# Kernel optimization log

Measured on AMD Instinct MI355X. Metric: run time of the kernel, lower is better.

## Reference

```python
import jax, jax.numpy as jnp
import numpy as np

BATCH = 64
IN_VECN = 1024
IN_VECL = 64
OUT_VECN = 64
OUT_VECL = 32
ROUTINGS = 3
EPS = 1e-5


def squash(x, axis=-1, eps=EPS):
    # squash(x) = |x|^2/(1+|x|^2) * x/(|x|+eps), matching the torch source
    n = jnp.linalg.norm(x, axis=axis, keepdims=True)
    n2 = n * n
    return n2 / (1.0 + n2) * x / (n + eps)


def setup_inputs() -> dict:
    key = jax.random.key(0)
    k1, k2, k3 = jax.random.split(key, 3)
    stdv = 1.0 / np.sqrt(IN_VECN * IN_VECL)  # reset_parameters: uniform(-stdv, stdv)
    u = jax.random.normal(k1, (BATCH, IN_VECN, IN_VECL), dtype=jnp.float32)
    weight = jax.random.uniform(k2, (IN_VECN, OUT_VECN, OUT_VECL, IN_VECL),
                                dtype=jnp.float32, minval=-stdv, maxval=stdv)
    bias = jax.random.uniform(k3, (IN_VECN, OUT_VECN, OUT_VECL),
                              dtype=jnp.float32, minval=-stdv, maxval=stdv)
    return {"u": u, "weight": weight, "bias": bias}


def reference(u, weight, bias):
    # u: [B, N, I]; weight: [N, O, L, I]; bias: [N, O, L]
    # u_hat: [B, N, O, L] -- per-input-capsule prediction for each output capsule
    u_hat = jnp.einsum('bni,noli->bnol', u, weight) + bias[None]
    # retain_grad=False: routing uses detached u_hat
    ud = jax.lax.stop_gradient(u_hat)
    # initial c = softmax(zeros) over out_vecn -> uniform 1/O, shape [1,1,O,1]
    c = jnp.full((1, 1, OUT_VECN, 1), 1.0 / OUT_VECN, dtype=u.dtype)
    b = jnp.zeros((u.shape[0], IN_VECN, OUT_VECN, 1), dtype=u.dtype)
    for _ in range(ROUTINGS - 1):
        v = squash(jnp.sum(ud * c, axis=-3), axis=-1)        # [B, O, L]
        b = b + jnp.sum(ud * v[:, None], axis=-1, keepdims=True)  # [B, N, O, 1]
        c = jax.nn.softmax(b, axis=-2)                        # softmax over O
    return squash(jnp.sum(u_hat * c, axis=-3), axis=-1)      # [B, O, L]
```

## Files before the change

kernel.cpp:

```cpp
#include <hip/hip_runtime.h>
#include <hip/hip_bf16.h>

#define BATCH 64
#define NIN 1024
#define IVL 64
#define ONUM 64
#define LVL 32
#define OLSZ 2048

typedef __attribute__((ext_vector_type(4))) float f32x4;
typedef __attribute__((ext_vector_type(8))) short short8;

static __device__ __forceinline__ unsigned short f2bf(float f) {
  unsigned u = __builtin_bit_cast(unsigned, f);
  u += 0x7fffu + ((u >> 16) & 1u);
  return (unsigned short)(u >> 16);
}
static __device__ __forceinline__ float bf2f_lo(unsigned x) {
  return __builtin_bit_cast(float, x << 16);
}
static __device__ __forceinline__ float bf2f_hi(unsigned x) {
  return __builtin_bit_cast(float, x & 0xffff0000u);
}

#define W_BURST(W, q0, q1, q2, q3)                                       \
  asm volatile(                                                          \
      "global_load_dwordx4 %[w0], %[a0], off\n\t"                        \
      "global_load_dwordx4 %[w1], %[a0], off offset:16\n\t"              \
      "global_load_dwordx4 %[w2], %[a0], off offset:128\n\t"             \
      "global_load_dwordx4 %[w3], %[a0], off offset:144\n\t"             \
      "global_load_dwordx4 %[w4], %[a1], off\n\t"                        \
      "global_load_dwordx4 %[w5], %[a1], off offset:16\n\t"              \
      "global_load_dwordx4 %[w6], %[a1], off offset:128\n\t"             \
      "global_load_dwordx4 %[w7], %[a1], off offset:144\n\t"             \
      "global_load_dwordx4 %[w8], %[a2], off\n\t"                        \
      "global_load_dwordx4 %[w9], %[a2], off offset:16\n\t"              \
      "global_load_dwordx4 %[w10], %[a2], off offset:128\n\t"            \
      "global_load_dwordx4 %[w11], %[a2], off offset:144\n\t"            \
      "global_load_dwordx4 %[w12], %[a3], off\n\t"                       \
      "global_load_dwordx4 %[w13], %[a3], off offset:16\n\t"             \
      "global_load_dwordx4 %[w14], %[a3], off offset:128\n\t"            \
      "global_load_dwordx4 %[w15], %[a3], off offset:144\n\t"            \
      : [w0] "=&v"(W[0]), [w1] "=&v"(W[1]), [w2] "=&v"(W[2]),            \
        [w3] "=&v"(W[3]), [w4] "=&v"(W[4]), [w5] "=&v"(W[5]),            \
        [w6] "=&v"(W[6]), [w7] "=&v"(W[7]), [w8] "=&v"(W[8]),            \
        [w9] "=&v"(W[9]), [w10] "=&v"(W[10]), [w11] "=&v"(W[11]),        \
        [w12] "=&v"(W[12]), [w13] "=&v"(W[13]), [w14] "=&v"(W[14]),      \
        [w15] "=&v"(W[15])                                               \
      : [a0] "v"(q0), [a1] "v"(q1), [a2] "v"(q2), [a3] "v"(q3)           \
      : "memory")

#define STORE16(P, s0, s1, s2, s3)                                       \
  asm volatile(                                                          \
      "global_store_dwordx2 %[a0], %[d0], off\n\t"                       \
      "global_store_dwordx2 %[a0], %[d1], off offset:32\n\t"             \
      "global_store_dwordx2 %[a0], %[d2], off offset:64\n\t"             \
      "global_store_dwordx2 %[a0], %[d3], off offset:96\n\t"             \
      "global_store_dwordx2 %[a1], %[d4], off\n\t"                       \
      "global_store_dwordx2 %[a1], %[d5], off offset:32\n\t"             \
      "global_store_dwordx2 %[a1], %[d6], off offset:64\n\t"             \
      "global_store_dwordx2 %[a1], %[d7], off offset:96\n\t"             \
      "global_store_dwordx2 %[a2], %[d8], off\n\t"                       \
      "global_store_dwordx2 %[a2], %[d9], off offset:32\n\t"             \
      "global_store_dwordx2 %[a2], %[d10], off offset:64\n\t"            \
      "global_store_dwordx2 %[a2], %[d11], off offset:96\n\t"            \
      "global_store_dwordx2 %[a3], %[d12], off\n\t"                      \
      "global_store_dwordx2 %[a3], %[d13], off offset:32\n\t"            \
      "global_store_dwordx2 %[a3], %[d14], off offset:64\n\t"            \
      "global_store_dwordx2 %[a3], %[d15], off offset:96\n\t"            \
      :: [a0] "v"(s0), [a1] "v"(s1), [a2] "v"(s2), [a3] "v"(s3),         \
         [d0] "v"(P[0]), [d1] "v"(P[1]), [d2] "v"(P[2]), [d3] "v"(P[3]), \
         [d4] "v"(P[4]), [d5] "v"(P[5]), [d6] "v"(P[6]), [d7] "v"(P[7]), \
         [d8] "v"(P[8]), [d9] "v"(P[9]), [d10] "v"(P[10]),               \
         [d11] "v"(P[11]), [d12] "v"(P[12]), [d13] "v"(P[13]),           \
         [d14] "v"(P[14]), [d15] "v"(P[15])                              \
      : "memory")

#define VMWAIT16                                        \
  do {                                                  \
    asm volatile("s_waitcnt vmcnt(16)" ::: "memory");   \
    __builtin_amdgcn_sched_barrier(0);                  \
  } while (0)
#define VMWAIT0                                         \
  do {                                                  \
    asm volatile("s_waitcnt vmcnt(0)" ::: "memory");    \
    __builtin_amdgcn_sched_barrier(0);                  \
  } while (0)

__global__ __launch_bounds__(256, 2) void k_gemm(
    const float* __restrict__ u, const float* __restrict__ w,
    const float* __restrict__ bias, unsigned short* __restrict__ uhat) {
  const int n = blockIdx.x;
  const int half = blockIdx.y;
  __shared__ __align__(16) unsigned short a_lds[64 * 72];
  __shared__ __align__(16) float bias_lds[1024];
  const int t = threadIdx.x;
  const int lane = t & 63;
  const int wave = t >> 6;
  const int row16 = lane & 15;
  const int quad = lane >> 4;

  {
    const int b = t >> 2;
    const int i0 = (t & 3) * 16;
    const float* src = u + (size_t)b * (NIN * IVL) + (size_t)n * IVL + i0;
    unsigned short* dst = a_lds + b * 72 + i0;
#pragma unroll
    for (int q = 0; q < 4; ++q) {
      float4 v = *(const float4*)(src + q * 4);
      dst[q * 4 + 0] = f2bf(v.x);
      dst[q * 4 + 1] = f2bf(v.y);
      dst[q * 4 + 2] = f2bf(v.z);
      dst[q * 4 + 3] = f2bf(v.w);
    }
    *(float4*)&bias_lds[t * 4] =
        *(const float4*)(bias + (size_t)n * OLSZ + half * 1024 + t * 4);
  }
  __syncthreads();

  short8 uf[4][2];
#pragma unroll
  for (int bt = 0; bt < 4; ++bt) {
#pragma unroll
    for (int ks = 0; ks < 2; ++ks) {
      uf[bt][ks] =
          *(const short8*)(a_lds + (bt * 16 + row16) * 72 + ks * 32 + quad * 8);
    }
  }
  asm volatile("s_waitcnt lgkmcnt(0)" ::: "memory");
  __builtin_amdgcn_sched_barrier(0);

  const float* wp = w + (size_t)n * (OLSZ * IVL) +
                    (size_t)(half * 1024 + wave * 64 + row16) * IVL + quad * 8;
  const float* p0 = wp;
  const float* p1 = wp + 16 * IVL;
  const float* p2 = wp + 32 * IVL;
  const float* p3 = wp + 48 * IVL;
  const unsigned short* sb0 =
      uhat + ((size_t)(0 * 16 + row16) * NIN + n) * OLSZ + half * 1024 +
      wave * 64 + quad * 4;
  const unsigned short* sb1 = sb0 + (size_t)16 * NIN * OLSZ;
  const unsigned short* sb2 = sb0 + (size_t)32 * NIN * OLSZ;
  const unsigned short* sb3 = sb0 + (size_t)48 * NIN * OLSZ;

  f32x4 wvA[16], wvB[16];

#define COMPUTE_STORE(W, c)                                                   \
  do {                                                                        \
    uint2 pks[16];                                                            \
    _Pragma("unroll") for (int tile = 0; tile < 4; ++tile) {                  \
      const f32x4 A0 = W[tile * 4 + 0];                                       \
      const f32x4 A1 = W[tile * 4 + 1];                                       \
      const f32x4 A2 = W[tile * 4 + 2];                                       \
      const f32x4 A3 = W[tile * 4 + 3];                                       \
      short8 wf0, wf1;                                                        \
      wf0[0] = (short)f2bf(A0[0]); wf0[1] = (short)f2bf(A0[1]);               \
      wf0[2] = (short)f2bf(A0[2]); wf0[3] = (short)f2bf(A0[3]);               \
      wf0[4] = (short)f2bf(A1[0]); wf0[5] = (short)f2bf(A1[1]);               \
      wf0[6] = (short)f2bf(A1[2]); wf0[7] = (short)f2bf(A1[3]);               \
      wf1[0] = (short)f2bf(A2[0]); wf1[1] = (short)f2bf(A2[1]);               \
      wf1[2] = (short)f2bf(A2[2]); wf1[3] = (short)f2bf(A2[3]);               \
      wf1[4] = (short)f2bf(A3[0]); wf1[5] = (short)f2bf(A3[1]);               \
      wf1[6] = (short)f2bf(A3[2]); wf1[7] = (short)f2bf(A3[3]);               \
      float4 bf = *(const float4*)&bias_lds[(c) * 256 + wave * 64 +           \
                                            tile * 16 + quad * 4];            \
      f32x4 acc0 = (f32x4){0.f, 0.f, 0.f, 0.f};                               \
      f32x4 acc1 = acc0, acc2 = acc0, acc3 = acc0;                            \
      acc0 = __builtin_amdgcn_mfma_f32_16x16x32_bf16(wf0, uf[0][0], acc0, 0, 0, 0); \
      acc0 = __builtin_amdgcn_mfma_f32_16x16x32_bf16(wf1, uf[0][1], acc0, 0, 0, 0); \
      acc1 = __builtin_amdgcn_mfma_f32_16x16x32_bf16(wf0, uf[1][0], acc1, 0, 0, 0); \
      acc1 = __builtin_amdgcn_mfma_f32_16x16x32_bf16(wf1, uf[1][1], acc1, 0, 0, 0); \
      acc2 = __builtin_amdgcn_mfma_f32_16x16x32_bf16(wf0, uf[2][0], acc2, 0, 0, 0); \
      acc2 = __builtin_amdgcn_mfma_f32_16x16x32_bf16(wf1, uf[2][1], acc2, 0, 0, 0); \
      acc3 = __builtin_amdgcn_mfma_f32_16x16x32_bf16(wf0, uf[3][0], acc3, 0, 0, 0); \
      acc3 = __builtin_amdgcn_mfma_f32_16x16x32_bf16(wf1, uf[3][1], acc3, 0, 0, 0); \
      pks[0 * 4 + tile] = make_uint2(                                         \
          f2bf(acc0[0] + bf.x) | (f2bf(acc0[1] + bf.y) << 16),                \
          f2bf(acc0[2] + bf.z) | (f2bf(acc0[3] + bf.w) << 16));               \
      pks[1 * 4 + tile] = make_uint2(                                         \
          f2bf(acc1[0] + bf.x) | (f2bf(acc1[1] + bf.y) << 16),                \
          f2bf(acc1[2] + bf.z) | (f2bf(acc1[3] + bf.w) << 16));               \
      pks[2 * 4 + tile] = make_uint2(                                         \
          f2bf(acc2[0] + bf.x) | (f2bf(acc2[1] + bf.y) << 16),                \
          f2bf(acc2[2] + bf.z) | (f2bf(acc2[3] + bf.w) << 16));               \
      pks[3 * 4 + tile] = make_uint2(                                         \
          f2bf(acc3[0] + bf.x) | (f2bf(acc3[1] + bf.y) << 16),                \
          f2bf(acc3[2] + bf.z) | (f2bf(acc3[3] + bf.w) << 16));               \
    }                                                                         \
    const unsigned short* s0 = sb0 + (c) * 256;                               \
    const unsigned short* s1 = sb1 + (c) * 256;                               \
    const unsigned short* s2 = sb2 + (c) * 256;                               \
    const unsigned short* s3 = sb3 + (c) * 256;                               \
    STORE16(pks, s0, s1, s2, s3);                                             \
  } while (0)

  W_BURST(wvA, p0, p1, p2, p3);
  W_BURST(wvB, p0 + 16384, p1 + 16384, p2 + 16384, p3 + 16384);
  VMWAIT16;
  COMPUTE_STORE(wvA, 0);
  W_BURST(wvA, p0 + 32768, p1 + 32768, p2 + 32768, p3 + 32768);
  VMWAIT16;
  COMPUTE_STORE(wvB, 1);
  W_BURST(wvB, p0 + 49152, p1 + 49152, p2 + 49152, p3 + 49152);
  VMWAIT16;
  COMPUTE_STORE(wvA, 2);
  VMWAIT0;
  COMPUTE_STORE(wvB, 3);
#undef COMPUTE_STORE
}

__global__ __launch_bounds__(256) void k_sum_n(
    const unsigned short* __restrict__ uhat, float* __restrict__ s1) {
  const int b = blockIdx.x >> 5;
  const int chunk = blockIdx.x & 31;
  const int t = threadIdx.x;
  const unsigned short* base =
      uhat + ((size_t)b * NIN + (size_t)chunk * 32) * OLSZ + t * 8;
  float acc[8];
#pragma unroll
  for (int j = 0; j < 8; ++j) acc[j] = 0.f;
#pragma unroll 4
  for (int k = 0; k < 32; ++k) {
    uint4 p = *(const uint4*)(base + (size_t)k * OLSZ);
    unsigned xs[4] = {p.x, p.y, p.z, p.w};
#pragma unroll
    for (int h = 0; h < 4; ++h) {
      acc[2 * h] += bf2f_lo(xs[h]);
      acc[2 * h + 1] += bf2f_hi(xs[h]);
    }
  }
  float* s = s1 + (size_t)b * OLSZ + t * 8;
#pragma unroll
  for (int j = 0; j < 8; ++j) atomicAdd(s + j, acc[j]);
}

__global__ __launch_bounds__(256) void k_route(
    const unsigned short* __restrict__ uhat, const float* __restrict__ sv,
    float scale, float* __restrict__ b1, int add_b1,
    float* __restrict__ sout) {
  const int b = blockIdx.x >> 5;
  const int chunk = blockIdx.x & 31;
  const int t = threadIdx.x;
  const int lane = t & 63;
  const int wave = t >> 6;
  const int g = lane >> 2;
  __shared__ float red[4][OLSZ];

  float v[4][8];
#pragma unroll
  for (int q = 0; q < 4; ++q) {
    const float* svp = sv + (size_t)b * OLSZ + q * 512 + lane * 8;
    float4 a0 = *(const float4*)svp;
    float4 a1 = *(const float4*)(svp + 4);
    v[q][0] = a0.x * scale; v[q][1] = a0.y * scale;
    v[q][2] = a0.z * scale; v[q][3] = a0.w * scale;
    v[q][4] = a1.x * scale; v[q][5] = a1.y * scale;
    v[q][6] = a1.z * scale; v[q][7] = a1.w * scale;
    float p = 0.f;
#pragma unroll
    for (int j = 0; j < 8; ++j) p = fmaf(v[q][j], v[q][j], p);
    p += __shfl_xor(p, 1);
    p += __shfl_xor(p, 2);
    float f = p / ((1.f + p) * (sqrtf(p) + 1e-5f));
#pragma unroll
    for (int j = 0; j < 8; ++j) v[q][j] *= f;
  }

  float racc[4][8];
#pragma unroll
  for (int q = 0; q < 4; ++q)
#pragma unroll
    for (int j = 0; j < 8; ++j) racc[q][j] = 0.f;

  const int n0 = chunk * 32 + wave * 8;
  const unsigned short* ub = uhat + ((size_t)b * NIN + n0) * OLSZ + lane * 8;

  uint4 pA[4], pB[4];
#pragma unroll
  for (int q = 0; q < 4; ++q) pA[q] = *(const uint4*)(ub + q * 512);

  auto process = [&](const uint4(&pk)[4], int k) {
    const int n = n0 + k;
    const size_t bbase = ((size_t)b * NIN + n) * ONUM + g;
    float b1v[4];
    if (add_b1) {
#pragma unroll
      for (int q = 0; q < 4; ++q) b1v[q] = b1[bbase + 16 * q];
    }
    float ud[4][8];
    float d[4];
#pragma unroll
    for (int q = 0; q < 4; ++q) {
      unsigned xs[4] = {pk[q].x, pk[q].y, pk[q].z, pk[q].w};
#pragma unroll
      for (int h = 0; h < 4; ++h) {
        ud[q][2 * h] = bf2f_lo(xs[h]);
        ud[q][2 * h + 1] = bf2f_hi(xs[h]);
      }
      float p = 0.f;
#pragma unroll
      for (int j = 0; j < 8; ++j) p = fmaf(ud[q][j], v[q][j], p);
      p += __shfl_xor(p, 1);
      p += __shfl_xor(p, 2);
      d[q] = p;
    }
    float bno[4];
    if (add_b1) {
#pragma unroll
      for (int q = 0; q < 4; ++q) bno[q] = d[q] + b1v[q];
    } else {
#pragma unroll
      for (int q = 0; q < 4; ++q) bno[q] = d[q];
      if ((lane & 3) == 0) {
#pragma unroll
        for (int q = 0; q < 4; ++q) b1[bbase + 16 * q] = d[q];
      }
    }
    float m = fmaxf(fmaxf(bno[0], bno[1]), fmaxf(bno[2], bno[3]));
#pragma unroll
    for (int dl = 4; dl < 64; dl <<= 1) m = fmaxf(m, __shfl_xor(m, dl));
    float e0 = __expf(bno[0] - m);
    float e1 = __expf(bno[1] - m);
    float e2 = __expf(bno[2] - m);
    float e3 = __expf(bno[3] - m);
    float ls = (e0 + e1) + (e2 + e3);
#pragma unroll
    for (int dl = 4; dl < 64; dl <<= 1) ls += __shfl_xor(ls, dl);
    float inv = 1.0f / ls;
    float c[4] = {e0 * inv, e1 * inv, e2 * inv, e3 * inv};
#pragma unroll
    for (int q = 0; q < 4; ++q) {
#pragma unroll
      for (int j = 0; j < 8; ++j)
        racc[q][j] = fmaf(c[q], ud[q][j], racc[q][j]);
    }
  };

#pragma unroll
  for (int kk = 0; kk < 4; ++kk) {
    {
#pragma unroll
      for (int q = 0; q < 4; ++q)
        pB[q] = *(const uint4*)(ub + (size_t)(2 * kk + 1) * OLSZ + q * 512);
    }
    process(pA, 2 * kk);
    if (2 * kk + 2 < 8) {
#pragma unroll
      for (int q = 0; q < 4; ++q)
        pA[q] = *(const uint4*)(ub + (size_t)(2 * kk + 2) * OLSZ + q * 512);
    }
    process(pB, 2 * kk + 1);
  }

#pragma unroll
  for (int q = 0; q < 4; ++q) {
    float* dst = &red[wave][q * 512 + lane * 8];
    *(float4*)(dst) =
        make_float4(racc[q][0], racc[q][1], racc[q][2], racc[q][3]);
    *(float4*)(dst + 4) =
        make_float4(racc[q][4], racc[q][5], racc[q][6], racc[q][7]);
  }
  __syncthreads();
  float* so = sout + (size_t)b * OLSZ;
#pragma unroll
  for (int j = 0; j < 8; ++j) {
    const int idx = t + 256 * j;
    float s = (red[0][idx] + red[1][idx]) + (red[2][idx] + red[3][idx]);
    atomicAdd(so + idx, s);
  }
}

__global__ __launch_bounds__(256) void k_final(const float* __restrict__ s3,
                                               float* __restrict__ out) {
  const int b = blockIdx.x;
  const int t = threadIdx.x;
  __shared__ float norm2[64];
  if (t < 64) norm2[t] = 0.f;
  __syncthreads();
  float scv[8];
#pragma unroll
  for (int k = 0; k < 8; ++k) {
    int idx = t + k * 256;
    float sc = s3[b * OLSZ + idx];
    scv[k] = sc;
    atomicAdd(&norm2[idx >> 5], sc * sc);
  }
  __syncthreads();
#pragma unroll
  for (int k = 0; k < 8; ++k) {
    int idx = t + k * 256;
    int o = idx >> 5;
    float n2 = norm2[o];
    float f = n2 / ((1.f + n2) * (sqrtf(n2) + 1e-5f));
    out[b * OLSZ + idx] = scv[k] * f;
  }
}

extern "C" void kernel_launch(void* const* d_in, const int* in_sizes, int n_in,
                              void* d_out, int out_size, void* d_ws,
                              size_t ws_size, hipStream_t stream) {
  const float* u = (const float*)d_in[0];
  const float* w = (const float*)d_in[1];
  const float* bias = (const float*)d_in[2];
  float* out = (float*)d_out;

  char* ws = (char*)d_ws;
  unsigned short* uhat = (unsigned short*)ws;
  float* b1 = (float*)(ws + (size_t)268435456);
  float* s1 = (float*)(ws + (size_t)268435456 + 16777216);
  float* s2 = s1 + 131072;
  float* s3 = s2 + 131072;

  hipMemsetAsync(s1, 0, 3 * 131072 * sizeof(float), stream);

  k_gemm<<<dim3(1024, 2), dim3(256), 0, stream>>>(u, w, bias, uhat);
  k_sum_n<<<dim3(2048), dim3(256), 0, stream>>>(uhat, s1);
  k_route<<<dim3(2048), dim3(256), 0, stream>>>(uhat, s1, 1.0f / 64.0f, b1, 0, s2);
  k_route<<<dim3(2048), dim3(256), 0, stream>>>(uhat, s2, 1.0f, b1, 1, s3);
  k_final<<<dim3(64), dim3(256), 0, stream>>>(s3, out);
}
```

Before: 492.1 us.

## Restructure GEMM weight pipeline into smaller bursts and fold memset into kernel

The gemm kernel now streams weights in 8-load bursts over eight double-buffered steps instead of 16-load bursts over four. Each wave now owns a contiguous 256-output span, so stores use immediate offsets from fixed base pointers. Weight prefetch is issued before the LDS barrier, and launch bounds rise to 3 blocks per CU to allow more concurrent waves. The memset of the accumulation buffers is removed and replaced by zeroing inside the gemm kernel, which saves one launch but relies on the buffers being zeroed before later kernels read them.

```diff
diff --git a/kernel.cpp b/kernel.cpp
--- a/kernel.cpp
+++ b/kernel.cpp
@@ -1,5 +1,4 @@
 #include <hip/hip_runtime.h>
-#include <hip/hip_bf16.h>
 
 #define BATCH 64
 #define NIN 1024
@@ -11,6 +10,9 @@
 typedef __attribute__((ext_vector_type(4))) float f32x4;
 typedef __attribute__((ext_vector_type(8))) short short8;
 
+#define STR_(x) #x
+#define STR(x) STR_(x)
+
 static __device__ __forceinline__ unsigned short f2bf(float f) {
   unsigned u = __builtin_bit_cast(unsigned, f);
   u += 0x7fffu + ((u >> 16) & 1u);
@@ -23,7 +25,7 @@
   return __builtin_bit_cast(float, x & 0xffff0000u);
 }
 
-#define W_BURST(W, q0, q1, q2, q3)                                       \
+#define W_BURST8(W, q0, q1)                                              \
   asm volatile(                                                          \
       "global_load_dwordx4 %[w0], %[a0], off\n\t"                        \
       "global_load_dwordx4 %[w1], %[a0], off offset:16\n\t"              \
@@ -33,122 +35,27 @@
       "global_load_dwordx4 %[w5], %[a1], off offset:16\n\t"              \
       "global_load_dwordx4 %[w6], %[a1], off offset:128\n\t"             \
       "global_load_dwordx4 %[w7], %[a1], off offset:144\n\t"             \
-      "global_load_dwordx4 %[w8], %[a2], off\n\t"                        \
-      "global_load_dwordx4 %[w9], %[a2], off offset:16\n\t"              \
-      "global_load_dwordx4 %[w10], %[a2], off offset:128\n\t"            \
-      "global_load_dwordx4 %[w11], %[a2], off offset:144\n\t"            \
-      "global_load_dwordx4 %[w12], %[a3], off\n\t"                       \
-      "global_load_dwordx4 %[w13], %[a3], off offset:16\n\t"             \
-      "global_load_dwordx4 %[w14], %[a3], off offset:128\n\t"            \
-      "global_load_dwordx4 %[w15], %[a3], off offset:144\n\t"            \
       : [w0] "=&v"(W[0]), [w1] "=&v"(W[1]), [w2] "=&v"(W[2]),            \
         [w3] "=&v"(W[3]), [w4] "=&v"(W[4]), [w5] "=&v"(W[5]),            \
-        [w6] "=&v"(W[6]), [w7] "=&v"(W[7]), [w8] "=&v"(W[8]),            \
-        [w9] "=&v"(W[9]), [w10] "=&v"(W[10]), [w11] "=&v"(W[11]),        \
-        [w12] "=&v"(W[12]), [w13] "=&v"(W[13]), [w14] "=&v"(W[14]),      \
-        [w15] "=&v"(W[15])                                               \
-      : [a0] "v"(q0), [a1] "v"(q1), [a2] "v"(q2), [a3] "v"(q3)           \
+        [w6] "=&v"(W[6]), [w7] "=&v"(W[7])                               \
+      : [a0] "v"(q0), [a1] "v"(q1)                                       \
       : "memory")
 
-#define STORE16(P, s0, s1, s2, s3)                                       \
-  asm volatile(                                                          \
-      "global_store_dwordx2 %[a0], %[d0], off\n\t"                       \
-      "global_store_dwordx2 %[a0], %[d1], off offset:32\n\t"             \
-      "global_store_dwordx2 %[a0], %[d2], off offset:64\n\t"             \
-      "global_store_dwordx2 %[a0], %[d3], off offset:96\n\t"             \
-      "global_store_dwordx2 %[a1], %[d4], off\n\t"                       \
-      "global_store_dwordx2 %[a1], %[d5], off offset:32\n\t"             \
-      "global_store_dwordx2 %[a1], %[d6], off offset:64\n\t"             \
-      "global_store_dwordx2 %[a1], %[d7], off offset:96\n\t"             \
-      "global_store_dwordx2 %[a2], %[d8], off\n\t"                       \
-      "global_store_dwordx2 %[a2], %[d9], off offset:32\n\t"             \
-      "global_store_dwordx2 %[a2], %[d10], off offset:64\n\t"            \
-      "global_store_dwordx2 %[a2], %[d11], off offset:96\n\t"            \
-      "global_store_dwordx2 %[a3], %[d12], off\n\t"                      \
-      "global_store_dwordx2 %[a3], %[d13], off offset:32\n\t"            \
-      "global_store_dwordx2 %[a3], %[d14], off offset:64\n\t"            \
-      "global_store_dwordx2 %[a3], %[d15], off offset:96\n\t"            \
-      :: [a0] "v"(s0), [a1] "v"(s1), [a2] "v"(s2), [a3] "v"(s3),         \
-         [d0] "v"(P[0]), [d1] "v"(P[1]), [d2] "v"(P[2]), [d3] "v"(P[3]), \
-         [d4] "v"(P[4]), [d5] "v"(P[5]), [d6] "v"(P[6]), [d7] "v"(P[7]), \
-         [d8] "v"(P[8]), [d9] "v"(P[9]), [d10] "v"(P[10]),               \
-         [d11] "v"(P[11]), [d12] "v"(P[12]), [d13] "v"(P[13]),           \
-         [d14] "v"(P[14]), [d15] "v"(P[15])                              \
-      : "memory")
-
-#define VMWAIT16                                        \
+#define VM_WAIT8                                        \
   do {                                                  \
-    asm volatile("s_waitcnt vmcnt(16)" ::: "memory");   \
+    asm volatile("s_waitcnt vmcnt(8)" ::: "memory");    \
     __builtin_amdgcn_sched_barrier(0);                  \
   } while (0)
-#define VMWAIT0                                         \
+#define VM_WAIT0                                        \
   do {                                                  \
     asm volatile("s_waitcnt vmcnt(0)" ::: "memory");    \
     __builtin_amdgcn_sched_barrier(0);                  \
   } while (0)
 
-__global__ __launch_bounds__(256, 2) void k_gemm(
-    const float* __restrict__ u, const float* __restrict__ w,
-    const float* __restrict__ bias, unsigned short* __restrict__ uhat) {
-  const int n = blockIdx.x;
-  const int half = blockIdx.y;
-  __shared__ __align__(16) unsigned short a_lds[64 * 72];
-  __shared__ __align__(16) float bias_lds[1024];
-  const int t = threadIdx.x;
-  const int lane = t & 63;
-  const int wave = t >> 6;
-  const int row16 = lane & 15;
-  const int quad = lane >> 4;
-
-  {
-    const int b = t >> 2;
-    const int i0 = (t & 3) * 16;
-    const float* src = u + (size_t)b * (NIN * IVL) + (size_t)n * IVL + i0;
-    unsigned short* dst = a_lds + b * 72 + i0;
-#pragma unroll
-    for (int q = 0; q < 4; ++q) {
-      float4 v = *(const float4*)(src + q * 4);
-      dst[q * 4 + 0] = f2bf(v.x);
-      dst[q * 4 + 1] = f2bf(v.y);
-      dst[q * 4 + 2] = f2bf(v.z);
-      dst[q * 4 + 3] = f2bf(v.w);
-    }
-    *(float4*)&bias_lds[t * 4] =
-        *(const float4*)(bias + (size_t)n * OLSZ + half * 1024 + t * 4);
-  }
-  __syncthreads();
-
-  short8 uf[4][2];
-#pragma unroll
-  for (int bt = 0; bt < 4; ++bt) {
-#pragma unroll
-    for (int ks = 0; ks < 2; ++ks) {
-      uf[bt][ks] =
-          *(const short8*)(a_lds + (bt * 16 + row16) * 72 + ks * 32 + quad * 8);
-    }
-  }
-  asm volatile("s_waitcnt lgkmcnt(0)" ::: "memory");
-  __builtin_amdgcn_sched_barrier(0);
-
-  const float* wp = w + (size_t)n * (OLSZ * IVL) +
-                    (size_t)(half * 1024 + wave * 64 + row16) * IVL + quad * 8;
-  const float* p0 = wp;
-  const float* p1 = wp + 16 * IVL;
-  const float* p2 = wp + 32 * IVL;
-  const float* p3 = wp + 48 * IVL;
-  const unsigned short* sb0 =
-      uhat + ((size_t)(0 * 16 + row16) * NIN + n) * OLSZ + half * 1024 +
-      wave * 64 + quad * 4;
-  const unsigned short* sb1 = sb0 + (size_t)16 * NIN * OLSZ;
-  const unsigned short* sb2 = sb0 + (size_t)32 * NIN * OLSZ;
-  const unsigned short* sb3 = sb0 + (size_t)48 * NIN * OLSZ;
-
-  f32x4 wvA[16], wvB[16];
-
-#define COMPUTE_STORE(W, c)                                                   \
+#define STEP(W, C, O0, O1)                                                    \
   do {                                                                        \
-    uint2 pks[16];                                                            \
-    _Pragma("unroll") for (int tile = 0; tile < 4; ++tile) {                  \
+    uint2 pks[8];                                                             \
+    _Pragma("unroll") for (int tile = 0; tile < 2; ++tile) {                  \
       const f32x4 A0 = W[tile * 4 + 0];                                       \
       const f32x4 A1 = W[tile * 4 + 1];                                       \
       const f32x4 A2 = W[tile * 4 + 2];                                       \
@@ -162,8 +69,8 @@
       wf1[2] = (short)f2bf(A2[2]); wf1[3] = (short)f2bf(A2[3]);               \
       wf1[4] = (short)f2bf(A3[0]); wf1[5] = (short)f2bf(A3[1]);               \
       wf1[6] = (short)f2bf(A3[2]); wf1[7] = (short)f2bf(A3[3]);               \
-      float4 bf = *(const float4*)&bias_lds[(c) * 256 + wave * 64 +           \
-                                            tile * 16 + quad * 4];            \
+      float4 bf = *(const float4*)&bias_lds[wave * 256 + (C)*32 + tile * 16 + \
+                                            quad * 4];                        \
       f32x4 acc0 = (f32x4){0.f, 0.f, 0.f, 0.f};                               \
       f32x4 acc1 = acc0, acc2 = acc0, acc3 = acc0;                            \
       acc0 = __builtin_amdgcn_mfma_f32_16x16x32_bf16(wf0, uf[0][0], acc0, 0, 0, 0); \
@@ -174,39 +81,104 @@
       acc2 = __builtin_amdgcn_mfma_f32_16x16x32_bf16(wf1, uf[2][1], acc2, 0, 0, 0); \
       acc3 = __builtin_amdgcn_mfma_f32_16x16x32_bf16(wf0, uf[3][0], acc3, 0, 0, 0); \
       acc3 = __builtin_amdgcn_mfma_f32_16x16x32_bf16(wf1, uf[3][1], acc3, 0, 0, 0); \
-      pks[0 * 4 + tile] = make_uint2(                                         \
+      pks[0 * 2 + tile] = make_uint2(                                         \
           f2bf(acc0[0] + bf.x) | (f2bf(acc0[1] + bf.y) << 16),                \
           f2bf(acc0[2] + bf.z) | (f2bf(acc0[3] + bf.w) << 16));               \
-      pks[1 * 4 + tile] = make_uint2(                                         \
+      pks[1 * 2 + tile] = make_uint2(                                         \
           f2bf(acc1[0] + bf.x) | (f2bf(acc1[1] + bf.y) << 16),                \
           f2bf(acc1[2] + bf.z) | (f2bf(acc1[3] + bf.w) << 16));               \
-      pks[2 * 4 + tile] = make_uint2(                                         \
+      pks[2 * 2 + tile] = make_uint2(                                         \
           f2bf(acc2[0] + bf.x) | (f2bf(acc2[1] + bf.y) << 16),                \
           f2bf(acc2[2] + bf.z) | (f2bf(acc2[3] + bf.w) << 16));               \
-      pks[3 * 4 + tile] = make_uint2(                                         \
+      pks[3 * 2 + tile] = make_uint2(                                         \
           f2bf(acc3[0] + bf.x) | (f2bf(acc3[1] + bf.y) << 16),                \
           f2bf(acc3[2] + bf.z) | (f2bf(acc3[3] + bf.w) << 16));               \
     }                                                                         \
-    const unsigned short* s0 = sb0 + (c) * 256;                               \
-    const unsigned short* s1 = sb1 + (c) * 256;                               \
-    const unsigned short* s2 = sb2 + (c) * 256;                               \
-    const unsigned short* s3 = sb3 + (c) * 256;                               \
-    STORE16(pks, s0, s1, s2, s3);                                             \
+    asm volatile(                                                             \
+        "global_store_dwordx2 %[a0], %[d0], off offset:" STR(O0) "\n\t"       \
+        "global_store_dwordx2 %[a0], %[d1], off offset:" STR(O1) "\n\t"       \
+        "global_store_dwordx2 %[a1], %[d2], off offset:" STR(O0) "\n\t"       \
+        "global_store_dwordx2 %[a1], %[d3], off offset:" STR(O1) "\n\t"       \
+        "global_store_dwordx2 %[a2], %[d4], off offset:" STR(O0) "\n\t"       \
+        "global_store_dwordx2 %[a2], %[d5], off offset:" STR(O1) "\n\t"       \
+        "global_store_dwordx2 %[a3], %[d6], off offset:" STR(O0) "\n\t"       \
+        "global_store_dwordx2 %[a3], %[d7], off offset:" STR(O1) "\n\t"       \
+        :: [a0] "v"(sb0), [a1] "v"(sb1), [a2] "v"(sb2), [a3] "v"(sb3),        \
+           [d0] "v"(pks[0]), [d1] "v"(pks[1]), [d2] "v"(pks[2]),              \
+           [d3] "v"(pks[3]), [d4] "v"(pks[4]), [d5] "v"(pks[5]),              \
+           [d6] "v"(pks[6]), [d7] "v"(pks[7])                                 \
+        : "memory");                                                          \
   } while (0)
 
-  W_BURST(wvA, p0, p1, p2, p3);
-  W_BURST(wvB, p0 + 16384, p1 + 16384, p2 + 16384, p3 + 16384);
-  VMWAIT16;
-  COMPUTE_STORE(wvA, 0);
-  W_BURST(wvA, p0 + 32768, p1 + 32768, p2 + 32768, p3 + 32768);
-  VMWAIT16;
-  COMPUTE_STORE(wvB, 1);
-  W_BURST(wvB, p0 + 49152, p1 + 49152, p2 + 49152, p3 + 49152);
-  VMWAIT16;
-  COMPUTE_STORE(wvA, 2);
-  VMWAIT0;
-  COMPUTE_STORE(wvB, 3);
-#undef COMPUTE_STORE
+__global__ __launch_bounds__(256, 3) void k_gemm(
+    const float* __restrict__ u, const float* __restrict__ w,
+    const float* __restrict__ bias, unsigned short* __restrict__ uhat,
+    float* __restrict__ szero) {
+  const int n = blockIdx.x;
+  const int half = blockIdx.y;
+  __shared__ __align__(16) unsigned short a_lds[64 * 72];
+  __shared__ __align__(16) float bias_lds[1024];
+  const int t = threadIdx.x;
+  const int lane = t & 63;
+  const int wave = t >> 6;
+  const int row16 = lane & 15;
+  const int quad = lane >> 4;
+
+  {
+    const int bid = blockIdx.y * gridDim.x + blockIdx.x;
+    if (t < 192) szero[bid * 192 + t] = 0.f;
+  }
+
+  {
+    const int b = t >> 2;
+    const int i0 = (t & 3) * 16;
+    const float* src = u + (size_t)b * (NIN * IVL) + (size_t)n * IVL + i0;
+    unsigned short* dst = a_lds + b * 72 + i0;
+#pragma unroll
+    for (int q = 0; q < 4; ++q) {
+      float4 v = *(const float4*)(src + q * 4);
+      dst[q * 4 + 0] = f2bf(v.x);
+      dst[q * 4 + 1] = f2bf(v.y);
+      dst[q * 4 + 2] = f2bf(v.z);
+      dst[q * 4 + 3] = f2bf(v.w);
+    }
+    *(float4*)&bias_lds[t * 4] =
+        *(const float4*)(bias + (size_t)n * OLSZ + half * 1024 + t * 4);
+  }
+
+  const float* wp = w + (size_t)n * (OLSZ * IVL) +
+                    (size_t)(half * 1024 + wave * 256 + row16) * IVL + quad * 8;
+  f32x4 bufA[8], bufB[8];
+  W_BURST8(bufA, wp, wp + 1024);
+  W_BURST8(bufB, wp + 2048, wp + 3072);
+
+  asm volatile("s_waitcnt lgkmcnt(0)" ::: "memory");
+  __builtin_amdgcn_s_barrier();
+
+  short8 uf[4][2];
+#pragma unroll
+  for (int bt = 0; bt < 4; ++bt) {
+#pragma unroll
+    for (int ks = 0; ks < 2; ++ks) {
+      uf[bt][ks] =
+          *(const short8*)(a_lds + (bt * 16 + row16) * 72 + ks * 32 + quad * 8);
+    }
+  }
+
+  const unsigned short* sb0 = uhat + ((size_t)row16 * NIN + n) * OLSZ +
+                              half * 1024 + wave * 256 + quad * 4;
+  const unsigned short* sb1 = sb0 + (size_t)16 * NIN * OLSZ;
+  const unsigned short* sb2 = sb0 + (size_t)32 * NIN * OLSZ;
+  const unsigned short* sb3 = sb0 + (size_t)48 * NIN * OLSZ;
+
+  VM_WAIT8; STEP(bufA, 0, 0, 32);    W_BURST8(bufA, wp + 4096,  wp + 5120);
+  VM_WAIT8; STEP(bufB, 1, 64, 96);   W_BURST8(bufB, wp + 6144,  wp + 7168);
+  VM_WAIT8; STEP(bufA, 2, 128, 160); W_BURST8(bufA, wp + 8192,  wp + 9216);
+  VM_WAIT8; STEP(bufB, 3, 192, 224); W_BURST8(bufB, wp + 10240, wp + 11264);
+  VM_WAIT8; STEP(bufA, 4, 256, 288); W_BURST8(bufA, wp + 12288, wp + 13312);
+  VM_WAIT8; STEP(bufB, 5, 320, 352); W_BURST8(bufB, wp + 14336, wp + 15360);
+  VM_WAIT8; STEP(bufA, 6, 384, 416);
+  VM_WAIT0; STEP(bufB, 7, 448, 480);
 }
 
 __global__ __launch_bounds__(256) void k_sum_n(
@@ -411,9 +383,7 @@
   float* s2 = s1 + 131072;
   float* s3 = s2 + 131072;
 
-  hipMemsetAsync(s1, 0, 3 * 131072 * sizeof(float), stream);
-
-  k_gemm<<<dim3(1024, 2), dim3(256), 0, stream>>>(u, w, bias, uhat);
+  k_gemm<<<dim3(1024, 2), dim3(256), 0, stream>>>(u, w, bias, uhat, s1);
   k_sum_n<<<dim3(2048), dim3(256), 0, stream>>>(uhat, s1);
   k_route<<<dim3(2048), dim3(256), 0, stream>>>(uhat, s1, 1.0f / 64.0f, b1, 0, s2);
   k_route<<<dim3(2048), dim3(256), 0, stream>>>(uhat, s2, 1.0f, b1, 1, s3);
```

Measured after the change: 529.0 us. 1.08x slower.
